# Optimization experiments

Measured on AMD Instinct MI355X. Metric: run time of the kernel, lower is better.

The kernel has to match this reference:

```python
import jax, jax.numpy as jnp
import numpy as np

NUM_HEADS = 32
NUM_KV_GROUPS = 8


def _rope(x, cos, sin):
    # x: [B, H, S, hd]; cos/sin: [S_max, hd]
    S, hd = x.shape[2], x.shape[3]
    x1, x2 = x[..., : hd // 2], x[..., hd // 2 :]
    rotated = jnp.concatenate((-x2, x1), axis=-1)
    c = cos[:S][None, None]
    s = sin[:S][None, None]
    return (x * c + rotated * s).astype(x.dtype)


def setup_inputs() -> dict:
    key = jax.random.key(0)
    ks = jax.random.split(key, 8)
    B, S, D = 2, 2048, 2048
    H, G = NUM_HEADS, NUM_KV_GROUPS
    hd = D // H
    scale = 1.0 / np.sqrt(D)
    return {
        "inputs": jax.random.normal(ks[0], (B, S, D), jnp.float32),
        "mask": jnp.zeros((S, S), jnp.bool_),  # note: original masked_fill is not in-place -> mask unused
        "cos": jax.random.uniform(ks[1], (S, hd), jnp.float32),
        "sin": jax.random.uniform(ks[2], (S, hd), jnp.float32),
        "Wq": jax.random.normal(ks[3], (D, H * hd), jnp.float32) * scale,
        "Wk": jax.random.normal(ks[4], (D, G * hd), jnp.float32) * scale,
        "Wv": jax.random.normal(ks[5], (D, G * hd), jnp.float32) * scale,
        "Wo": jax.random.normal(ks[6], (H * hd, H * hd), jnp.float32) * scale,
    }


def reference(inputs, mask, cos, sin, Wq, Wk, Wv, Wo):
    B, S, D = inputs.shape
    H, G = NUM_HEADS, NUM_KV_GROUPS
    hd = Wq.shape[1] // H
    group_size = H // G

    q = (inputs @ Wq).reshape(B, S, H, hd).transpose(0, 2, 1, 3)  # [B,H,S,hd]
    k = (inputs @ Wk).reshape(B, S, G, hd).transpose(0, 2, 1, 3)  # [B,G,S,hd]
    v = (inputs @ Wv).reshape(B, S, G, hd).transpose(0, 2, 1, 3)

    q = _rope(q, cos, sin)
    k = _rope(k, cos, sin)

    k = jnp.repeat(k, group_size, axis=1)  # [B,H,S,hd]
    v = jnp.repeat(v, group_size, axis=1)

    scores = jnp.einsum("bhqd,bhkd->bhqk", q, k)
    # NOTE: original uses non-inplace masked_fill whose result is discarded,
    # so faithfully NO mask is applied.
    attn = jax.nn.softmax(scores / jnp.sqrt(jnp.float32(hd)).astype(scores.dtype), axis=-1)
    ctx = jnp.einsum("bhqk,bhkd->bhqd", attn, v)
    ctx = ctx.transpose(0, 2, 1, 3).reshape(B, S, H * hd)
    return ctx @ Wo
```

## Files before the change

### kernel.cpp

```cpp
#include <hip/hip_runtime.h>
#include <stdint.h>

typedef __attribute__((ext_vector_type(8))) short short8;
typedef __attribute__((ext_vector_type(4))) short short4v;
typedef __attribute__((ext_vector_type(4))) float float4v;
typedef __attribute__((ext_vector_type(2))) unsigned uint2v;

__device__ __forceinline__ float bf2f(short s) {
  union { unsigned u; float f; } x;
  x.u = ((unsigned)(unsigned short)s) << 16;
  return x.f;
}
__device__ __forceinline__ short f2bf(float f) {
  union { float f; unsigned u; } x;
  x.f = f;
  unsigned r = x.u + 0x7fffu + ((x.u >> 16) & 1u);
  return (short)(r >> 16);
}
__device__ __forceinline__ void glds16(const void* g, void* l) {
  __builtin_amdgcn_global_load_lds(
      (const __attribute__((address_space(1))) void*)g,
      (__attribute__((address_space(3))) void*)l, 16, 0, 0);
}

__global__ __launch_bounds__(256) void f32_to_bf16(const float* __restrict__ s,
                                                   short* __restrict__ d) {
  const long i = ((long)blockIdx.x * 256 + threadIdx.x) * 8;
  const float4v a = *(const float4v*)&s[i];
  const float4v b = *(const float4v*)&s[i + 4];
  short8 v;
#pragma unroll
  for (int e = 0; e < 4; ++e) { v[e] = f2bf(a[e]); v[e + 4] = f2bf(b[e]); }
  *(short8*)&d[i] = v;
}

__global__ __launch_bounds__(256) void transpose_f2b(
    const float* __restrict__ src, short* __restrict__ dst, int R, int C) {
  __shared__ short t[64 * 72];
  const int tid = threadIdx.x;
  const int r0 = blockIdx.y * 64, c0 = blockIdx.x * 64;
#pragma unroll
  for (int r = 0; r < 2; ++r) {
    int c = r * 256 + tid;
    int row = c >> 3, col8 = (c & 7) * 8;
    const float4v a = *(const float4v*)&src[(long)(r0 + row) * C + c0 + col8];
    const float4v b = *(const float4v*)&src[(long)(r0 + row) * C + c0 + col8 + 4];
    short8 v;
#pragma unroll
    for (int e = 0; e < 4; ++e) { v[e] = f2bf(a[e]); v[e + 4] = f2bf(b[e]); }
    *(short8*)&t[row * 72 + col8] = v;
  }
  __syncthreads();
#pragma unroll
  for (int r = 0; r < 2; ++r) {
    int c = r * 256 + tid;
    int orow = c >> 3, ocol8 = (c & 7) * 8;
    short8 w;
#pragma unroll
    for (int e = 0; e < 8; ++e) w[e] = t[(ocol8 + e) * 72 + orow];
    *(short8*)&dst[(long)(c0 + orow) * R + r0 + ocol8] = w;
  }
}

__global__ __launch_bounds__(256) void vtrans(const short* __restrict__ Y,
                                              short* __restrict__ Vt,
                                              int ld, int col0) {
  const int bg = blockIdx.y;
  const int b = bg >> 3, gk = bg & 7;
  const int s0 = blockIdx.x * 64;
  __shared__ short t[64 * 72];
  const int tid = threadIdx.x;
#pragma unroll
  for (int r = 0; r < 2; ++r) {
    int c = r * 256 + tid;
    int row = c >> 3, col8 = (c & 7) * 8;
    short8 v = *(const short8*)&Y[(long)(b * 2048 + s0 + row) * ld + col0 + gk * 64 + col8];
    *(short8*)&t[row * 72 + col8] = v;
  }
  __syncthreads();
#pragma unroll
  for (int r = 0; r < 2; ++r) {
    int c = r * 256 + tid;
    int d = c >> 3, s8 = (c & 7) * 8;
    short8 w;
#pragma unroll
    for (int e = 0; e < 8; ++e) w[e] = t[(s8 + e) * 72 + d];
    *(short8*)&Vt[((long)bg * 64 + d) * 2048 + s0 + s8] = w;
  }
}

__global__ __launch_bounds__(256) void rope_kernel(
    const short* __restrict__ Y, const float* __restrict__ cosp,
    const float* __restrict__ sinp, short* __restrict__ out,
    int NH, int lgNH, int ld, int col0, float scale) {
  const long tid = (long)blockIdx.x * 256 + threadIdx.x;
  const int d = (int)(tid & 31);
  const long t1 = tid >> 5;
  const int h = (int)(t1 & (NH - 1));
  const long t2 = t1 >> lgNH;
  const int s = (int)(t2 & 2047);
  const int b = (int)(t2 >> 11);
  const long ib = (long)(b * 2048 + s) * ld + col0 + h * 64 + d;
  const float x1 = bf2f(Y[ib]);
  const float x2 = bf2f(Y[ib + 32]);
  const float c1 = cosp[s * 64 + d];
  const float c2 = cosp[s * 64 + d + 32];
  const float s1 = sinp[s * 64 + d];
  const float s2 = sinp[s * 64 + d + 32];
  const long ob = ((long)(b * NH + h) * 2048 + s) * 64 + d;
  out[ob] = f2bf((x1 * c1 - x2 * s1) * scale);
  out[ob + 32] = f2bf((x2 * c2 + x1 * s2) * scale);
}

template <typename OutT>
__global__ __launch_bounds__(256) void gemm_bt(
    const short* __restrict__ A, const short* __restrict__ BT,
    OutT* __restrict__ C, int M, int N, int K) {
  __shared__ short As[128 * 32];
  __shared__ short Bs[128 * 32];
  const int tid = threadIdx.x;
  const int wave = tid >> 6, lane = tid & 63;
  const int g = lane >> 4, lr = lane & 15;
  const int m0 = blockIdx.y * 128, n0 = blockIdx.x * 128;
  const int wr = wave >> 1, wc = wave & 1;

  float4v acc[4][4];
#pragma unroll
  for (int i = 0; i < 4; ++i)
#pragma unroll
    for (int j = 0; j < 4; ++j) acc[i][j] = (float4v)0.f;

  for (int kt = 0; kt < K; kt += 32) {
#pragma unroll
    for (int r = 0; r < 2; ++r) {
      const int cb = r * 256 + wave * 64;
      const int c = cb + lane;
      const int row = c >> 2, kc = c & 3;
      glds16(A + (long)(m0 + row) * K + kt + kc * 8, As + cb * 8);
      glds16(BT + (long)(n0 + row) * K + kt + kc * 8, Bs + cb * 8);
    }
    __syncthreads();
    short8 af[4], bfr[4];
#pragma unroll
    for (int i = 0; i < 4; ++i)
      af[i] = *(const short8*)&As[(wr * 64 + i * 16 + lr) * 32 + g * 8];
#pragma unroll
    for (int j = 0; j < 4; ++j)
      bfr[j] = *(const short8*)&Bs[(wc * 64 + j * 16 + lr) * 32 + g * 8];
#pragma unroll
    for (int i = 0; i < 4; ++i)
#pragma unroll
      for (int j = 0; j < 4; ++j)
        acc[i][j] = __builtin_amdgcn_mfma_f32_16x16x32_bf16(af[i], bfr[j], acc[i][j], 0, 0, 0);
    __syncthreads();
  }

#pragma unroll
  for (int i = 0; i < 4; ++i)
#pragma unroll
    for (int j = 0; j < 4; ++j)
#pragma unroll
      for (int t = 0; t < 4; ++t) {
        const int r = m0 + wr * 64 + i * 16 + g * 4 + t;
        const int cc = n0 + wc * 64 + j * 16 + lr;
        float v = acc[i][j][t];
        if constexpr (sizeof(OutT) == 2)
          C[(long)r * N + cc] = f2bf(v);
        else
          C[(long)r * N + cc] = v;
      }
}

__global__ __launch_bounds__(512, 2) void attn_kernel(
    const short* __restrict__ Qr, const short* __restrict__ Kr,
    const short* __restrict__ Vt, short* __restrict__ Ctx) {
  constexpr int S = 2048;
  const int bh = blockIdx.y;
  const int b = bh >> 5, h = bh & 31;
  const int gk = h >> 2;
  const int q0 = blockIdx.x << 7;
  const int tid = threadIdx.x;
  const int w = tid >> 6, lane = tid & 63;
  const int g = lane >> 4, lr = lane & 15;
  const int b8 = lr & 7;
  const int qrow = w * 16 + lr;

  __shared__ short Ks[128 * 64];
  __shared__ short Vs[64 * 128];
  __shared__ short Ps[128 * 128];

  const short* Qb = Qr + (long)(b * 32 + h) * S * 64;
  const short* KbIt = Kr + (long)(b * 8 + gk) * S * 64;
  const short* VbIt = Vt + (long)(b * 8 + gk) * 64 * S;

  const int ko0 = lr * 64 + ((0 + g) ^ b8) * 8;
  const int ko1 = lr * 64 + ((4 + g) ^ b8) * 8;
  const int jv0 = g ^ b8;
  const int vo0 = lr * 128 + jv0 * 8;
  const int vo1 = lr * 128 + (jv0 ^ 4) * 8;
  int pr[4], pw[8];
#pragma unroll
  for (int ks = 0; ks < 4; ++ks) pr[ks] = qrow * 128 + ((4 * ks + g) ^ b8) * 8;
#pragma unroll
  for (int i = 0; i < 8; ++i)
    pw[i] = qrow * 128 + ((2 * i + (g >> 1)) ^ b8) * 8 + (g & 1) * 4;

  long koff[2], voff[2];
#pragma unroll
  for (int r = 0; r < 2; ++r) {
    const int c = r * 512 + w * 64 + lane;
    const int kv = c >> 3, slot = c & 7;
    koff[r] = (long)kv * 64 + (slot ^ (kv & 7)) * 8;
    const int dd = c >> 4, s16 = c & 15;
    voff[r] = (long)dd * S + ((s16 & 8) | ((s16 & 7) ^ (dd & 7))) * 8;
  }

  short8 qf[2];
  qf[0] = *(const short8*)&Qb[(long)(q0 + qrow) * 64 + g * 8];
  qf[1] = *(const short8*)&Qb[(long)(q0 + qrow) * 64 + 32 + g * 8];

  float4v rs4 = (float4v)0.f;
  float4v oacc[4];
#pragma unroll
  for (int di = 0; di < 4; ++di) oacc[di] = (float4v)0.f;

  for (int it = 0; it < 16; ++it) {
#pragma unroll
    for (int r = 0; r < 2; ++r) {
      const int cb = r * 512 + w * 64;
      glds16(KbIt + koff[r], Ks + cb * 8);
      glds16(VbIt + voff[r], Vs + cb * 8);
    }
    __syncthreads();

    float4v sacc[8];
#pragma unroll
    for (int i = 0; i < 8; ++i) sacc[i] = (float4v)0.f;
#pragma unroll
    for (int i = 0; i < 8; ++i) {
      const short8 a0 = *(const short8*)&Ks[ko0 + i * 1024];
      sacc[i] = __builtin_amdgcn_mfma_f32_16x16x32_bf16(a0, qf[0], sacc[i], 0, 0, 0);
    }
#pragma unroll
    for (int i = 0; i < 8; ++i) {
      const short8 a1 = *(const short8*)&Ks[ko1 + i * 1024];
      sacc[i] = __builtin_amdgcn_mfma_f32_16x16x32_bf16(a1, qf[1], sacc[i], 0, 0, 0);
    }

#pragma unroll
    for (int i = 0; i < 8; ++i) {
      union { float f; unsigned u; } a0, a1, a2, a3;
      a0.f = exp2f(sacc[i][0]);
      a1.f = exp2f(sacc[i][1]);
      a2.f = exp2f(sacc[i][2]);
      a3.f = exp2f(sacc[i][3]);
      rs4[0] += a0.f; rs4[1] += a1.f; rs4[2] += a2.f; rs4[3] += a3.f;
      const unsigned d0 = __builtin_amdgcn_perm(a1.u + 0x8000u, a0.u + 0x8000u, 0x07060302u);
      const unsigned d1 = __builtin_amdgcn_perm(a3.u + 0x8000u, a2.u + 0x8000u, 0x07060302u);
      *(uint2v*)&Ps[pw[i]] = (uint2v){d0, d1};
    }

#pragma unroll
    for (int ks = 0; ks < 4; ++ks) {
      const short8 pf = *(const short8*)&Ps[pr[ks]];
      const int vbase = (ks & 1) ? vo1 : vo0;
#pragma unroll
      for (int di = 0; di < 4; ++di) {
        const short8 vf = *(const short8*)&Vs[vbase + di * 2048 + (ks >> 1) * 64];
        oacc[di] = __builtin_amdgcn_mfma_f32_16x16x32_bf16(vf, pf, oacc[di], 0, 0, 0);
      }
    }
    __syncthreads();
    KbIt += 128 * 64;
    VbIt += 128;
  }

  float rs = rs4[0] + rs4[1] + rs4[2] + rs4[3];
  rs += __shfl_xor(rs, 16, 64);
  rs += __shfl_xor(rs, 32, 64);
  const float inv = 1.f / rs;

  const int q = q0 + qrow;
#pragma unroll
  for (int di = 0; di < 4; ++di) {
    short4v o;
#pragma unroll
    for (int t = 0; t < 4; ++t) o[t] = f2bf(oacc[di][t] * inv);
    *(short4v*)&Ctx[(long)(b * S + q) * 2048 + h * 64 + di * 16 + g * 4] = o;
  }
}

extern "C" void kernel_launch(void* const* d_in, const int* in_sizes, int n_in,
                              void* d_out, int out_size, void* d_ws, size_t ws_size,
                              hipStream_t stream) {
  (void)in_sizes; (void)n_in; (void)out_size; (void)ws_size;
  const float* X    = (const float*)d_in[0];
  const float* cosp = (const float*)d_in[2];
  const float* sinp = (const float*)d_in[3];
  const float* Wq   = (const float*)d_in[4];
  const float* Wk   = (const float*)d_in[5];
  const float* Wv   = (const float*)d_in[6];
  const float* Wo   = (const float*)d_in[7];
  float* out = (float*)d_out;
  char* ws = (char*)d_ws;

  short* Xb = (short*)(ws + 0);
  short* WT = (short*)(ws + 16777216);
  short* Y  = (short*)(ws + 29360128);
  short* Qr = (short*)(ws + 54525952);
  short* Kr = (short*)(ws + 71303168);
  short* Vt = (short*)(ws + 75497472);

  f32_to_bf16<<<4096, 256, 0, stream>>>(X, Xb);
  transpose_f2b<<<dim3(32, 32), 256, 0, stream>>>(Wq, WT, 2048, 2048);
  transpose_f2b<<<dim3(8, 32), 256, 0, stream>>>(Wk, WT + 2048 * 2048, 2048, 512);
  transpose_f2b<<<dim3(8, 32), 256, 0, stream>>>(Wv, WT + 2560 * 2048, 2048, 512);

  gemm_bt<short><<<dim3(24, 32), 256, 0, stream>>>(Xb, WT, Y, 4096, 3072, 2048);

  transpose_f2b<<<dim3(32, 32), 256, 0, stream>>>(Wo, WT, 2048, 2048);

  rope_kernel<<<16384, 256, 0, stream>>>(Y, cosp, sinp, Qr, 32, 5, 3072, 0, 0.18033688011112043f);
  rope_kernel<<<4096, 256, 0, stream>>>(Y, cosp, sinp, Kr, 8, 3, 3072, 2048, 1.0f);
  vtrans<<<dim3(32, 16), 256, 0, stream>>>(Y, Vt, 3072, 2560);

  attn_kernel<<<dim3(16, 64), 512, 0, stream>>>(Qr, Kr, Vt, Y);

  gemm_bt<float><<<dim3(16, 32), 256, 0, stream>>>(Y, WT, out, 4096, 2048, 2048);
}
```

Before: 395.9 us.

## Compute softmax row sums via MFMA, use native exp2, merge weight transposes

The attention kernel now gets each row's softmax denominator from an extra MFMA that multiplies the bf16 probability tile by a ones vector. This replaces the per-element float adds and the cross-lane shuffles. The sum is now taken over bf16-rounded probabilities, which also keeps it consistent with the numerator. exp2f is swapped for the hardware v_exp_f32 intrinsic to avoid the libm range handling. The three Q/K/V weight-transpose launches are folded into one 3D launch, where out-of-range blocks exit early, to save launch overhead.

Result: faster. 379.6 us (-4.1%).

```diff
diff --git a/kernel.cpp b/kernel.cpp
--- a/kernel.cpp
+++ b/kernel.cpp
@@ -16,6 +16,15 @@
   x.f = f;
   unsigned r = x.u + 0x7fffu + ((x.u >> 16) & 1u);
   return (short)(r >> 16);
+}
+__device__ __forceinline__ float fexp2(float x) {
+#if __has_builtin(__builtin_amdgcn_exp2f)
+  return __builtin_amdgcn_exp2f(x);
+#else
+  float r;
+  asm("v_exp_f32 %0, %1" : "=v"(r) : "v"(x));
+  return r;
+#endif
 }
 __device__ __forceinline__ void glds16(const void* g, void* l) {
   __builtin_amdgcn_global_load_lds(
@@ -34,11 +43,11 @@
   *(short8*)&d[i] = v;
 }
 
-__global__ __launch_bounds__(256) void transpose_f2b(
-    const float* __restrict__ src, short* __restrict__ dst, int R, int C) {
+__device__ __forceinline__ void transpose_tile(
+    const float* __restrict__ src, short* __restrict__ dst, int R, int C,
+    int r0, int c0) {
   __shared__ short t[64 * 72];
   const int tid = threadIdx.x;
-  const int r0 = blockIdx.y * 64, c0 = blockIdx.x * 64;
 #pragma unroll
   for (int r = 0; r < 2; ++r) {
     int c = r * 256 + tid;
@@ -60,6 +69,22 @@
     for (int e = 0; e < 8; ++e) w[e] = t[(ocol8 + e) * 72 + orow];
     *(short8*)&dst[(long)(c0 + orow) * R + r0 + ocol8] = w;
   }
+}
+
+__global__ __launch_bounds__(256) void transpose_f2b(
+    const float* __restrict__ src, short* __restrict__ dst, int R, int C) {
+  transpose_tile(src, dst, R, C, blockIdx.y * 64, blockIdx.x * 64);
+}
+
+__global__ __launch_bounds__(256) void wtrans3(
+    const float* __restrict__ Wq, const float* __restrict__ Wk,
+    const float* __restrict__ Wv, short* __restrict__ WT) {
+  const int z = blockIdx.z;
+  const float* src = z == 0 ? Wq : (z == 1 ? Wk : Wv);
+  const int C = z == 0 ? 2048 : 512;
+  if (blockIdx.x * 64 >= C) return;
+  short* dst = WT + (z == 0 ? 0 : (z == 1 ? 2048 * 2048 : 2560 * 2048));
+  transpose_tile(src, dst, 2048, C, blockIdx.y * 64, blockIdx.x * 64);
 }
 
 __global__ __launch_bounds__(256) void vtrans(const short* __restrict__ Y,
@@ -219,7 +244,8 @@
   qf[0] = *(const short8*)&Qb[(long)(q0 + qrow) * 64 + g * 8];
   qf[1] = *(const short8*)&Qb[(long)(q0 + qrow) * 64 + 32 + g * 8];
 
-  float4v rs4 = (float4v)0.f;
+  const short8 ones = (short8)(short)0x3F80;
+  float4v lacc = (float4v)0.f;
   float4v oacc[4];
 #pragma unroll
   for (int di = 0; di < 4; ++di) oacc[di] = (float4v)0.f;
@@ -250,11 +276,10 @@
 #pragma unroll
     for (int i = 0; i < 8; ++i) {
       union { float f; unsigned u; } a0, a1, a2, a3;
-      a0.f = exp2f(sacc[i][0]);
-      a1.f = exp2f(sacc[i][1]);
-      a2.f = exp2f(sacc[i][2]);
-      a3.f = exp2f(sacc[i][3]);
-      rs4[0] += a0.f; rs4[1] += a1.f; rs4[2] += a2.f; rs4[3] += a3.f;
+      a0.f = fexp2(sacc[i][0]);
+      a1.f = fexp2(sacc[i][1]);
+      a2.f = fexp2(sacc[i][2]);
+      a3.f = fexp2(sacc[i][3]);
       const unsigned d0 = __builtin_amdgcn_perm(a1.u + 0x8000u, a0.u + 0x8000u, 0x07060302u);
       const unsigned d1 = __builtin_amdgcn_perm(a3.u + 0x8000u, a2.u + 0x8000u, 0x07060302u);
       *(uint2v*)&Ps[pw[i]] = (uint2v){d0, d1};
@@ -264,6 +289,7 @@
     for (int ks = 0; ks < 4; ++ks) {
       const short8 pf = *(const short8*)&Ps[pr[ks]];
       const int vbase = (ks & 1) ? vo1 : vo0;
+      lacc = __builtin_amdgcn_mfma_f32_16x16x32_bf16(ones, pf, lacc, 0, 0, 0);
 #pragma unroll
       for (int di = 0; di < 4; ++di) {
         const short8 vf = *(const short8*)&Vs[vbase + di * 2048 + (ks >> 1) * 64];
@@ -275,10 +301,7 @@
     VbIt += 128;
   }
 
-  float rs = rs4[0] + rs4[1] + rs4[2] + rs4[3];
-  rs += __shfl_xor(rs, 16, 64);
-  rs += __shfl_xor(rs, 32, 64);
-  const float inv = 1.f / rs;
+  const float inv = 1.f / lacc[0];
 
   const int q = q0 + qrow;
 #pragma unroll
@@ -312,9 +335,7 @@
   short* Vt = (short*)(ws + 75497472);
 
   f32_to_bf16<<<4096, 256, 0, stream>>>(X, Xb);
-  transpose_f2b<<<dim3(32, 32), 256, 0, stream>>>(Wq, WT, 2048, 2048);
-  transpose_f2b<<<dim3(8, 32), 256, 0, stream>>>(Wk, WT + 2048 * 2048, 2048, 512);
-  transpose_f2b<<<dim3(8, 32), 256, 0, stream>>>(Wv, WT + 2560 * 2048, 2048, 512);
+  wtrans3<<<dim3(32, 32, 3), 256, 0, stream>>>(Wq, Wk, Wv, WT);
 
   gemm_bt<short><<<dim3(24, 32), 256, 0, stream>>>(Xb, WT, Y, 4096, 3072, 2048);
 
```
